# Kernel tuning notes

Hardware: AMD Instinct MI355X
Metric: run time of the kernel (lower is better)

Reference implementation:

```python
import jax, jax.numpy as jnp
import numpy as np

LMAX = 5
RESOLUTION = 12
ASPECT_RATIO = 2
BATCH = 256
NB = 2 * RESOLUTION                       # res_beta = 24
NA = round(2 * ASPECT_RATIO * RESOLUTION)  # res_alpha = res_gamma = 48
DIM = sum((2 * l + 1) ** 2 for l in range(LMAX + 1))  # 286

# normalize2mom constant for tanh: (E_{z~N(0,1)}[tanh(z)^2])^{-1/2}
_x = np.linspace(-12.0, 12.0, 1_000_001)
_pdf = np.exp(-0.5 * _x * _x) / np.sqrt(2.0 * np.pi)
ACT_CST = float(np.trapz(np.tanh(_x) ** 2 * _pdf, _x) ** -0.5)  # ~1.5927


def _su2_generators(j):
    m = np.arange(-j, j)
    raising = np.diag(-np.sqrt(j * (j + 1) - m * (m + 1)), k=-1).astype(complex)
    m = np.arange(-j + 1, j + 1)
    lowering = np.diag(np.sqrt(j * (j + 1) - m * (m - 1)), k=1).astype(complex)
    m = np.arange(-j, j + 1)
    return np.stack([0.5 * (raising + lowering), np.diag(1j * m), -0.5j * (raising - lowering)])


def _q_real_to_complex(l):
    q = np.zeros((2 * l + 1, 2 * l + 1), dtype=complex)
    for m in range(-l, 0):
        q[l + m, l + abs(m)] = 1 / np.sqrt(2)
        q[l + m, l - abs(m)] = -1j / np.sqrt(2)
    q[l, l] = 1
    for m in range(1, l + 1):
        q[l + m, l + abs(m)] = (-1) ** m / np.sqrt(2)
        q[l + m, l - abs(m)] = 1j * (-1) ** m / np.sqrt(2)
    return (-1j) ** l * q


def _so3_generators(l):
    X = _su2_generators(l)
    Q = _q_real_to_complex(l)
    return np.real(np.conj(Q.T)[None] @ X @ Q[None])  # real [3, 2l+1, 2l+1]


def _expm_angles(A, t):
    """exp(t_n * A) for real antisymmetric A via eigendecomposition. -> [n, d, d] real"""
    vals, vecs = np.linalg.eig(A.astype(complex))
    inv = np.linalg.inv(vecs)
    phases = np.exp(t[:, None] * vals[None, :])  # [n, d]
    return np.real(np.einsum('ij,nj,jk->nik', vecs, phases, inv))


def _build_D_and_qw():
    # Euler angle grids (e3nn SO3Grid convention)
    b = (np.arange(NB) + 0.5) / NB * np.pi          # beta   [nb]
    a = np.arange(NA) / NA * 2.0 * np.pi            # alpha=gamma [na]
    blocks = []
    for l in range(LMAX + 1):
        X = _so3_generators(l)
        Ra = _expm_angles(X[1], a)   # exp(alpha * X1)  [na,d,d]
        Rb = _expm_angles(X[0], b)   # exp(beta  * X0)  [nb,d,d]
        # D^l(a,b,c) = Ra[a] @ Rb[b] @ Ra[c]
        Dl = np.einsum('xij,yjk,zkl->xyzil', Ra, Rb, Ra)
        blocks.append(np.sqrt(2 * l + 1) * Dl.reshape(NA, NB, NA, -1))
    D = np.concatenate(blocks, axis=-1).astype(np.float32)  # [na, nb, na, dim]
    # lie_learn / Kostelec-Rockmore quadrature weights for beta
    bb = NB // 2
    k = np.arange(bb)
    j = np.arange(2 * bb)
    w = (2.0 / bb) * np.sin(np.pi * (2 * j + 1) / (4.0 * bb)) * np.sum(
        (1.0 / (2 * k + 1))[None, :]
        * np.sin((2 * j[:, None] + 1) * (2 * k[None, :] + 1) * np.pi / (4.0 * bb)),
        axis=1,
    )
    w = w / (2.0 * (2 * bb) ** 2)
    qw = (w * NB ** 2 / NA ** 2).astype(np.float32)  # [nb]
    return jnp.asarray(D), jnp.asarray(qw)


def setup_inputs() -> dict:
    key = jax.random.key(0)
    features = jax.random.normal(key, (BATCH, DIM), dtype=jnp.float32)
    D, qw = _build_D_and_qw()
    return {"features": features, "D": D, "qw": qw}


def reference(features, D, qw):
    dim = D.shape[-1]
    s = jnp.sqrt(jnp.asarray(dim, features.dtype))
    # to_grid: [B, dim] x [na, nb, na, dim] -> [B, na, nb, na]
    g = jnp.einsum('bi,xyzi->bxyz', features, D) / s
    # normalized pointwise nonlinearity on SO(3) samples
    g = ACT_CST * jnp.tanh(g)
    # from_grid: quadrature-weighted projection back onto flat Wigner basis
    return jnp.einsum('bxyz,y,xyzi->bi', g, qw, D) * s
```

## Files before the change

kernel.cpp:

```cpp
#include <hip/hip_runtime.h>
#include <hip/hip_bf16.h>

#define DIM    286
#define DIMP   288
#define NZTOT  55296
#define NBATCH 256
#define NB_    24
#define NA_    48
#define ZC     32
#define NTILES 1728
#define NCHUNK 192
#define TILES_PER_WG 9
#define S_CONST 16.911534525287763f
#define INV_S   0.05913123959890826f
#define ACT_CST 1.5927f
#define TWO_LOG2E 2.8853900817779268f

typedef short bf16x8 __attribute__((ext_vector_type(8)));
typedef float f32x4  __attribute__((ext_vector_type(4)));

#define WS_FBF  0u
#define WS_DBF  147456u
#define WS_DT   (WS_DBF + 31850496u)
#define WS_PART (WS_DT + 31850496u)

typedef const __attribute__((address_space(1))) char GA;
typedef __attribute__((address_space(3))) char LA;
__device__ __forceinline__ void gload_lds16(const void* g, void* l) {
    __builtin_amdgcn_global_load_lds((GA*)g, (LA*)l, 16, 0, 0);
}

__global__ void k_prep(const float* __restrict__ F, const float* __restrict__ D,
                       const float* __restrict__ qw,
                       __hip_bfloat16* __restrict__ Fbf,
                       __hip_bfloat16* __restrict__ Dbf, __hip_bfloat16* __restrict__ Dt2) {
    __shared__ __align__(16) float T[9152];
    __shared__ float qs[24];
    int t = threadIdx.x;
    int bid = blockIdx.x;
    if (bid >= NTILES) {
        int o = (bid - NTILES) * 256 + t;
        int row = o / DIMP, col = o % DIMP;
        float v = (col < DIM) ? F[row * DIM + col] * INV_S : 0.f;
        Fbf[o] = __float2bfloat16(v);
        return;
    }
    int z0 = bid * 32;
    if (t < 24) qs[t] = qw[t] * S_CONST;
    {
        int wave = t >> 6, lane = t & 63;
        const char* src = (const char*)(D + (size_t)z0 * DIM);
        char* dst = (char*)T;
        #pragma unroll
        for (int j = 0; j < 9; ++j) {
            int c = wave + j * 4;
            if (c < 35 || (c == 35 && lane < 48))
                gload_lds16(src + c * 1024 + lane * 16, dst + c * 1024);
        }
    }
    asm volatile("s_waitcnt vmcnt(0)" ::: "memory");
    __syncthreads();
    for (int m = 0; m < 18; ++m) {
        int d = t + m * 256;
        int z = d / 144, i2 = d % 144;
        int i = i2 * 2;
        __hip_bfloat162 o2;
        if (i < DIM) {
            float2 v = *(const float2*)(&T[z * DIM + i]);
            o2.x = __float2bfloat16(v.x); o2.y = __float2bfloat16(v.y);
        } else {
            o2.x = __float2bfloat16(0.f); o2.y = o2.x;
        }
        *(__hip_bfloat162*)(Dbf + (size_t)(z0 + z) * DIMP + i) = o2;
    }
    for (int s = 0; s < 5; ++s) {
        int idx = t + s * 256;
        if (idx < 1152) {
            int i = idx >> 2, zc = idx & 3;
            __hip_bfloat16 o8[8];
            #pragma unroll
            for (int j = 0; j < 8; ++j) {
                int zl = zc * 8 + j;
                int y = ((z0 + zl) / NA_) % NB_;
                o8[j] = __float2bfloat16(T[zl * DIM + i] * qs[y]);
            }
            *(bf16x8*)(Dt2 + ((size_t)bid * DIMP + i) * ZC + zc * 8) = *(const bf16x8*)o8;
        }
    }
}

__launch_bounds__(256, 2)
__global__ void k_main(const __hip_bfloat16* __restrict__ Fbf,
                       const __hip_bfloat16* __restrict__ Dbf,
                       const __hip_bfloat16* __restrict__ Dt2,
                       __hip_bfloat16* __restrict__ part) {
    __shared__ __align__(16) __hip_bfloat16 Ds[32][288];
    __shared__ __align__(16) __hip_bfloat16 Dts[288][32];
    __shared__ __align__(16) __hip_bfloat16 Gs[4][32][32];

    int t = threadIdx.x;
    int wave = t >> 6, lane = t & 63, ln = lane & 15, q = lane >> 4;

    bf16x8 fa[2][9];
    int rowbase = blockIdx.y * 128 + wave * 32;
    #pragma unroll
    for (int h = 0; h < 2; ++h) {
        const __hip_bfloat16* fp = Fbf + (size_t)(rowbase + h * 16 + ln) * DIMP + q * 8;
        #pragma unroll
        for (int ks = 0; ks < 9; ++ks) fa[h][ks] = *(const bf16x8*)(fp + ks * 32);
    }

    f32x4 acc[2][18];
    #pragma unroll
    for (int h = 0; h < 2; ++h)
        #pragma unroll
        for (int n = 0; n < 18; ++n) acc[h][n] = (f32x4){0.f, 0.f, 0.f, 0.f};

    #pragma unroll 1
    for (int k = 0; k < TILES_PER_WG; ++k) {
        int tz = blockIdx.x * TILES_PER_WG + k;
        {
            const char* src; char* dst;
            if (wave < 2) {
                src = (const char*)(Dbf + (size_t)tz * ZC * DIMP) + wave * 9216 + lane * 16;
                dst = ((char*)&Ds[0][0]) + wave * 9216;
            } else {
                src = (const char*)(Dt2 + (size_t)tz * DIMP * ZC) + (wave - 2) * 9216 + lane * 16;
                dst = ((char*)&Dts[0][0]) + (wave - 2) * 9216;
            }
            #pragma unroll
            for (int j = 0; j < 9; ++j)
                gload_lds16(src + j * 1024, dst + j * 1024);
        }
        asm volatile("s_waitcnt vmcnt(0)" ::: "memory");
        __syncthreads();
        f32x4 g00 = (f32x4){0.f,0.f,0.f,0.f}, g01 = (f32x4){0.f,0.f,0.f,0.f};
        f32x4 g10 = (f32x4){0.f,0.f,0.f,0.f}, g11 = (f32x4){0.f,0.f,0.f,0.f};
        #pragma unroll
        for (int ks = 0; ks < 9; ++ks) {
            bf16x8 b0 = *(const bf16x8*)(&Ds[ln][ks * 32 + q * 8]);
            bf16x8 b1 = *(const bf16x8*)(&Ds[16 + ln][ks * 32 + q * 8]);
            g00 = __builtin_amdgcn_mfma_f32_16x16x32_bf16(fa[0][ks], b0, g00, 0, 0, 0);
            g01 = __builtin_amdgcn_mfma_f32_16x16x32_bf16(fa[0][ks], b1, g01, 0, 0, 0);
            g10 = __builtin_amdgcn_mfma_f32_16x16x32_bf16(fa[1][ks], b0, g10, 0, 0, 0);
            g11 = __builtin_amdgcn_mfma_f32_16x16x32_bf16(fa[1][ks], b1, g11, 0, 0, 0);
        }
        #pragma unroll
        for (int h = 0; h < 2; ++h) {
            #pragma unroll
            for (int zh = 0; zh < 2; ++zh) {
                f32x4 g = (h == 0) ? (zh == 0 ? g00 : g01) : (zh == 0 ? g10 : g11);
                #pragma unroll
                for (int r = 0; r < 4; ++r) {
                    float x = g[r];
                    float a = fabsf(x);
                    float e = __builtin_amdgcn_exp2f(-TWO_LOG2E * a);
                    float v = ACT_CST - 2.f * ACT_CST * e * __builtin_amdgcn_rcpf(1.f + e);
                    v = copysignf(v, x);
                    Gs[wave][h * 16 + q * 4 + r][zh * 16 + ln] = __float2bfloat16(v);
                }
            }
        }
        bf16x8 a20 = *(const bf16x8*)(&Gs[wave][ln][q * 8]);
        bf16x8 a21 = *(const bf16x8*)(&Gs[wave][16 + ln][q * 8]);
        #pragma unroll
        for (int nf = 0; nf < 18; ++nf) {
            bf16x8 b2 = *(const bf16x8*)(&Dts[nf * 16 + ln][q * 8]);
            acc[0][nf] = __builtin_amdgcn_mfma_f32_16x16x32_bf16(a20, b2, acc[0][nf], 0, 0, 0);
            acc[1][nf] = __builtin_amdgcn_mfma_f32_16x16x32_bf16(a21, b2, acc[1][nf], 0, 0, 0);
        }
        __syncthreads();
    }
    __hip_bfloat16* pw = part + (size_t)blockIdx.x * (NBATCH * DIMP)
                       + ((size_t)blockIdx.y * 128 + wave * 32) * DIMP;
    #pragma unroll
    for (int h = 0; h < 2; ++h) {
        #pragma unroll
        for (int m = 0; m < 9; ++m) {
            __hip_bfloat16 o8[8];
            #pragma unroll
            for (int j = 0; j < 8; ++j)
                o8[j] = __float2bfloat16(acc[h][2 * m + (j >> 2)][j & 3]);
            *(bf16x8*)(pw + (size_t)((h * 9 + m) * 64 + lane) * 8) = *(const bf16x8*)o8;
        }
    }
}

__global__ void k_reduce(const __hip_bfloat16* __restrict__ part, float* __restrict__ out) {
    __shared__ float red[3][16][8];
    int t = threadIdx.x, wave = t >> 6, lane = t & 63;
    int j = lane & 15;
    int zg = wave * 4 + (lane >> 4);
    int s = blockIdx.x * 16 + j;
    const __hip_bfloat16* p = part + (size_t)s * 8;
    float sum[8];
    #pragma unroll
    for (int kk = 0; kk < 8; ++kk) sum[kk] = 0.f;
    #pragma unroll 4
    for (int ii = 0; ii < 12; ++ii) {
        bf16x8 v = *(const bf16x8*)(p + (size_t)(zg * 12 + ii) * (NBATCH * DIMP));
        #pragma unroll
        for (int kk = 0; kk < 8; ++kk) {
            __hip_bfloat16 h; *(short*)&h = v[kk];
            sum[kk] += __bfloat162float(h);
        }
    }
    #pragma unroll
    for (int kk = 0; kk < 8; ++kk) {
        sum[kk] += __shfl_down(sum[kk], 16);
        sum[kk] += __shfl_down(sum[kk], 32);
    }
    if (wave > 0 && lane < 16) {
        #pragma unroll
        for (int kk = 0; kk < 8; ++kk) red[wave - 1][lane][kk] = sum[kk];
    }
    __syncthreads();
    if (wave == 0 && lane < 16) {
        #pragma unroll
        for (int w = 0; w < 3; ++w)
            #pragma unroll
            for (int kk = 0; kk < 8; ++kk) sum[kk] += red[w][lane][kk];
        int wr = s / 1152, si = s % 1152;
        int lane_m = si % 64, m9 = si / 64;
        int h = m9 / 9, m = m9 % 9, q = lane_m >> 4, ln = lane_m & 15;
        int rowb = wr * 32 + h * 16 + q * 4;
        #pragma unroll
        for (int j8 = 0; j8 < 8; ++j8) {
            int nf = 2 * m + (j8 >> 2), r = j8 & 3;
            int i = nf * 16 + ln;
            if (i < DIM) out[(rowb + r) * DIM + i] = sum[j8];
        }
    }
}

extern "C" void kernel_launch(void* const* d_in, const int* in_sizes, int n_in,
                              void* d_out, int out_size, void* d_ws, size_t ws_size,
                              hipStream_t stream) {
    const float* F  = (const float*)d_in[0];
    const float* D  = (const float*)d_in[1];
    const float* qw = (const float*)d_in[2];
    char* ws = (char*)d_ws;
    __hip_bfloat16* Fbf = (__hip_bfloat16*)(ws + WS_FBF);
    __hip_bfloat16* Dbf = (__hip_bfloat16*)(ws + WS_DBF);
    __hip_bfloat16* Dt2 = (__hip_bfloat16*)(ws + WS_DT);
    __hip_bfloat16* part = (__hip_bfloat16*)(ws + WS_PART);

    k_prep<<<NTILES + 288, 256, 0, stream>>>(F, D, qw, Fbf, Dbf, Dt2);
    k_main<<<dim3(NCHUNK, 2), 256, 0, stream>>>(Fbf, Dbf, Dt2, part);
    k_reduce<<<576, 256, 0, stream>>>(part, (float*)d_out);
}
```

Baseline: 139.6 us.

## Swizzle LDS tile layouts and rebalance tiles over more workgroup chunks

Prep now writes D tiles to global memory in an XOR-swizzled chunk layout, so the direct global-to-LDS copies land in a bank-conflict-free arrangement. The main kernel reads Ds, Dts and Gs through matching swizzled offsets. The z-tiles are also split across 256 chunks (7 or 6 tiles each) instead of 192 chunks of 9, for better CU occupancy. The cost is more partial sums for the reduce kernel to add up, and offset logic that must stay consistent between prep and main.

```diff
diff --git a/kernel.cpp b/kernel.cpp
--- a/kernel.cpp
+++ b/kernel.cpp
@@ -9,8 +9,7 @@
 #define NA_    48
 #define ZC     32
 #define NTILES 1728
-#define NCHUNK 192
-#define TILES_PER_WG 9
+#define NCHUNK 256
 #define S_CONST 16.911534525287763f
 #define INV_S   0.05913123959890826f
 #define ACT_CST 1.5927f
@@ -60,6 +59,7 @@
     }
     asm volatile("s_waitcnt vmcnt(0)" ::: "memory");
     __syncthreads();
+    char* dbB = (char*)Dbf + (size_t)bid * 18432;
     for (int m = 0; m < 18; ++m) {
         int d = t + m * 256;
         int z = d / 144, i2 = d % 144;
@@ -71,8 +71,10 @@
         } else {
             o2.x = __float2bfloat16(0.f); o2.y = o2.x;
         }
-        *(__hip_bfloat162*)(Dbf + (size_t)(z0 + z) * DIMP + i) = o2;
-    }
+        int off = (((i >> 5) * 2048) + z * 64 + (i & 31) * 2) ^ ((z & 7) << 4);
+        *(__hip_bfloat162*)(dbB + off) = o2;
+    }
+    char* dtB = (char*)Dt2 + (size_t)bid * 18432;
     for (int s = 0; s < 5; ++s) {
         int idx = t + s * 256;
         if (idx < 1152) {
@@ -84,7 +86,8 @@
                 int y = ((z0 + zl) / NA_) % NB_;
                 o8[j] = __float2bfloat16(T[zl * DIM + i] * qs[y]);
             }
-            *(bf16x8*)(Dt2 + ((size_t)bid * DIMP + i) * ZC + zc * 8) = *(const bf16x8*)o8;
+            int off = (i * 64 + zc * 16) ^ ((i & 7) << 4);
+            *(bf16x8*)(dtB + off) = *(const bf16x8*)o8;
         }
     }
 }
@@ -94,12 +97,14 @@
                        const __hip_bfloat16* __restrict__ Dbf,
                        const __hip_bfloat16* __restrict__ Dt2,
                        __hip_bfloat16* __restrict__ part) {
-    __shared__ __align__(16) __hip_bfloat16 Ds[32][288];
-    __shared__ __align__(16) __hip_bfloat16 Dts[288][32];
-    __shared__ __align__(16) __hip_bfloat16 Gs[4][32][32];
+    __shared__ __align__(16) char DsB[18432];
+    __shared__ __align__(16) char DtB[18432];
+    __shared__ __align__(16) char GsB[8192];
 
     int t = threadIdx.x;
     int wave = t >> 6, lane = t & 63, ln = lane & 15, q = lane >> 4;
+    int xsw = (ln & 7) << 4;
+    int cA = (ln * 64 + q * 16) ^ xsw;
 
     bf16x8 fa[2][9];
     int rowbase = blockIdx.y * 128 + wave * 32;
@@ -116,17 +121,21 @@
         #pragma unroll
         for (int n = 0; n < 18; ++n) acc[h][n] = (f32x4){0.f, 0.f, 0.f, 0.f};
 
+    int bx = blockIdx.x;
+    int tstart = (bx < 192) ? bx * 7 : bx * 6 + 192;
+    int ntile = (bx < 192) ? 7 : 6;
+
     #pragma unroll 1
-    for (int k = 0; k < TILES_PER_WG; ++k) {
-        int tz = blockIdx.x * TILES_PER_WG + k;
+    for (int k = 0; k < ntile; ++k) {
+        int tz = tstart + k;
         {
             const char* src; char* dst;
             if (wave < 2) {
-                src = (const char*)(Dbf + (size_t)tz * ZC * DIMP) + wave * 9216 + lane * 16;
-                dst = ((char*)&Ds[0][0]) + wave * 9216;
+                src = (const char*)Dbf + (size_t)tz * 18432 + wave * 9216 + lane * 16;
+                dst = DsB + wave * 9216;
             } else {
-                src = (const char*)(Dt2 + (size_t)tz * DIMP * ZC) + (wave - 2) * 9216 + lane * 16;
-                dst = ((char*)&Dts[0][0]) + (wave - 2) * 9216;
+                src = (const char*)Dt2 + (size_t)tz * 18432 + (wave - 2) * 9216 + lane * 16;
+                dst = DtB + (wave - 2) * 9216;
             }
             #pragma unroll
             for (int j = 0; j < 9; ++j)
@@ -138,8 +147,8 @@
         f32x4 g10 = (f32x4){0.f,0.f,0.f,0.f}, g11 = (f32x4){0.f,0.f,0.f,0.f};
         #pragma unroll
         for (int ks = 0; ks < 9; ++ks) {
-            bf16x8 b0 = *(const bf16x8*)(&Ds[ln][ks * 32 + q * 8]);
-            bf16x8 b1 = *(const bf16x8*)(&Ds[16 + ln][ks * 32 + q * 8]);
+            bf16x8 b0 = *(const bf16x8*)(DsB + ks * 2048 + cA);
+            bf16x8 b1 = *(const bf16x8*)(DsB + ks * 2048 + 1024 + cA);
             g00 = __builtin_amdgcn_mfma_f32_16x16x32_bf16(fa[0][ks], b0, g00, 0, 0, 0);
             g01 = __builtin_amdgcn_mfma_f32_16x16x32_bf16(fa[0][ks], b1, g01, 0, 0, 0);
             g10 = __builtin_amdgcn_mfma_f32_16x16x32_bf16(fa[1][ks], b0, g10, 0, 0, 0);
@@ -157,15 +166,17 @@
                     float e = __builtin_amdgcn_exp2f(-TWO_LOG2E * a);
                     float v = ACT_CST - 2.f * ACT_CST * e * __builtin_amdgcn_rcpf(1.f + e);
                     v = copysignf(v, x);
-                    Gs[wave][h * 16 + q * 4 + r][zh * 16 + ln] = __float2bfloat16(v);
+                    int row = h * 16 + q * 4 + r;
+                    int goff = (wave << 11) + ((row * 64 + (zh * 16 + ln) * 2) ^ ((row & 7) << 4));
+                    *(__hip_bfloat16*)(GsB + goff) = __float2bfloat16(v);
                 }
             }
         }
-        bf16x8 a20 = *(const bf16x8*)(&Gs[wave][ln][q * 8]);
-        bf16x8 a21 = *(const bf16x8*)(&Gs[wave][16 + ln][q * 8]);
+        bf16x8 a20 = *(const bf16x8*)(GsB + (wave << 11) + cA);
+        bf16x8 a21 = *(const bf16x8*)(GsB + (wave << 11) + 1024 + cA);
         #pragma unroll
         for (int nf = 0; nf < 18; ++nf) {
-            bf16x8 b2 = *(const bf16x8*)(&Dts[nf * 16 + ln][q * 8]);
+            bf16x8 b2 = *(const bf16x8*)(DtB + nf * 1024 + cA);
             acc[0][nf] = __builtin_amdgcn_mfma_f32_16x16x32_bf16(a20, b2, acc[0][nf], 0, 0, 0);
             acc[1][nf] = __builtin_amdgcn_mfma_f32_16x16x32_bf16(a21, b2, acc[1][nf], 0, 0, 0);
         }
@@ -197,8 +208,8 @@
     #pragma unroll
     for (int kk = 0; kk < 8; ++kk) sum[kk] = 0.f;
     #pragma unroll 4
-    for (int ii = 0; ii < 12; ++ii) {
-        bf16x8 v = *(const bf16x8*)(p + (size_t)(zg * 12 + ii) * (NBATCH * DIMP));
+    for (int ii = 0; ii < 16; ++ii) {
+        bf16x8 v = *(const bf16x8*)(p + (size_t)(zg * 16 + ii) * (NBATCH * DIMP));
         #pragma unroll
         for (int kk = 0; kk < 8; ++kk) {
             __hip_bfloat16 h; *(short*)&h = v[kk];
```

New measurement: 151.4 us. 8.4% more time.
